# Optimization experiments

Measured on AMD Instinct MI355X. Metric: run time of the kernel, lower is better.

The kernel has to match this reference:

```python
import jax, jax.numpy as jnp
import numpy as np

DIM = 512
TEMB_DIM = 512
NUM_HEADS = 16
WS = 16  # window_size
N = WS * WS
B = 256


def _relative_position_index(ws: int) -> np.ndarray:
    """Swin-style relative position index, shape [ws*ws, ws*ws], values in [0, (2ws-1)^2)."""
    coords = np.stack(np.meshgrid(np.arange(ws), np.arange(ws), indexing='ij'))  # [2, ws, ws]
    flat = coords.reshape(2, -1)                                                  # [2, N]
    rel = flat[:, :, None] - flat[:, None, :]                                     # [2, N, N]
    rel = rel.transpose(1, 2, 0).copy()                                           # [N, N, 2]
    rel[:, :, 0] += ws - 1
    rel[:, :, 1] += ws - 1
    rel[:, :, 0] *= 2 * ws - 1
    return rel.sum(-1).astype(np.int32)


def setup_inputs() -> dict:
    key = jax.random.key(0)
    ks = jax.random.split(key, 8)
    lin = lambda k, fan_in, shape: jax.random.normal(k, shape, jnp.float32) * (1.0 / np.sqrt(fan_in))
    return {
        'x': jax.random.normal(ks[0], (B, N, DIM), jnp.float32),
        'temb': jax.random.normal(ks[1], (B, TEMB_DIM), jnp.float32),
        'qkv_w': lin(ks[2], DIM, (DIM, 3 * DIM)),
        'qkv_b': jnp.zeros((3 * DIM,), jnp.float32),
        'temb_w': lin(ks[3], TEMB_DIM, (TEMB_DIM, 3 * DIM)),
        'temb_b': jnp.zeros((3 * DIM,), jnp.float32),
        'rpb_table': jax.random.normal(ks[4], ((2 * WS - 1) ** 2, NUM_HEADS), jnp.float32) * 0.02,
        'proj_w': lin(ks[5], DIM, (DIM, DIM)),
        'proj_b': jnp.zeros((DIM,), jnp.float32),
        'rp_index': jnp.asarray(_relative_position_index(WS)),
    }


def reference(x, temb, qkv_w, qkv_b, temb_w, temb_b, rpb_table, proj_w, proj_b, rp_index):
    Bq, Nq, C = x.shape
    H = NUM_HEADS
    hd = C // H
    # qkv with time-embedding modulation: [B, N, 3C]
    qkv = x @ qkv_w + qkv_b + (temb @ temb_w + temb_b)[:, None, :]
    qkv = qkv.reshape(Bq, Nq, 3, H, hd).transpose(2, 0, 3, 1, 4)  # [3, B, H, N, hd]
    q, k, v = qkv[0], qkv[1], qkv[2]
    # relative position bias: [H, N, N]
    bias = rpb_table[rp_index.reshape(-1)].reshape(Nq, Nq, H).transpose(2, 0, 1)
    scale = 1.0 / jnp.sqrt(jnp.asarray(hd, x.dtype))  # SDPA default scale
    scores = jnp.einsum('bhqd,bhkd->bhqk', q, k) * scale + bias[None]
    attn = jax.nn.softmax(scores, axis=-1)
    out = jnp.einsum('bhqk,bhkd->bhqd', attn, v)       # [B, H, N, hd]
    out = out.transpose(0, 2, 1, 3).reshape(Bq, Nq, C)
    return out @ proj_w + proj_b
```

## Files before the change

### kernel.cpp

```cpp
#include <hip/hip_runtime.h>
#include <hip/hip_bf16.h>

#define B_ 256
#define N_ 256
#define H_ 16
#define SCALE2_ 0.25504526484f
#define LOG2E_ 1.4426950408889634f

typedef __attribute__((ext_vector_type(8))) short short8;
typedef __attribute__((ext_vector_type(4))) float f32x4v;
typedef unsigned int u32;

#define GLOAD16(gptr, lptr)                                                        \
  __builtin_amdgcn_global_load_lds((const __attribute__((address_space(1))) u32*)(gptr), \
                                   (__attribute__((address_space(3))) u32*)(lptr), 16, 0, 0)

static __device__ __forceinline__ unsigned cvt_pk_bf16(float lo, float hi) {
  unsigned r;
  asm("v_cvt_pk_bf16_f32 %0, %1, %2" : "=v"(r) : "v"(lo), "v"(hi));
  return r;
}

__global__ __launch_bounds__(512)
void prep_kernel(const float* __restrict__ temb, const float* __restrict__ temb_w,
                 const float* __restrict__ temb_b, const float* __restrict__ qkv_b,
                 float* __restrict__ tm,
                 const float* __restrict__ x, unsigned* __restrict__ xb16,
                 const float* __restrict__ qkv_w, unsigned short* __restrict__ qkv_wT,
                 const float* __restrict__ proj_w, unsigned short* __restrict__ proj_wT) {
  __shared__ __align__(16) char lbuf[17024];
  const int blk = blockIdx.x;
  const int t = threadIdx.x;

  if (blk < 256) {
    float* ts = (float*)lbuf;
    const int b = blk;
    ts[t] = temb[(size_t)b * 512 + t];
    __syncthreads();
    float a0 = temb_b[t] + qkv_b[t];
    float a1 = temb_b[t + 512] + qkv_b[t + 512];
    float a2 = temb_b[t + 1024] + qkv_b[t + 1024];
#pragma unroll 4
    for (int k = 0; k < 512; ++k) {
      const float tv = ts[k];
      const float* wr = temb_w + (size_t)k * 1536 + t;
      a0 += tv * wr[0];
      a1 += tv * wr[512];
      a2 += tv * wr[1024];
    }
    float* o = tm + (size_t)b * 1536 + t;
    o[0] = a0; o[512] = a1; o[1024] = a2;
  } else if (blk < 1280) {
    const int n8 = (B_ * N_ * 512) / 8;
    int i = (blk - 256) * 512 + t;
    for (; i < n8; i += 1024 * 512) {
      const float4* p = reinterpret_cast<const float4*>(x + (size_t)i * 8);
      float4 a = p[0], b4 = p[1];
      uint4 vv = make_uint4(cvt_pk_bf16(a.x, a.y), cvt_pk_bf16(a.z, a.w),
                            cvt_pk_bf16(b4.x, b4.y), cvt_pk_bf16(b4.z, b4.w));
      *reinterpret_cast<uint4*>(xb16 + (size_t)i * 4) = vv;
    }
  } else {
    const float* src; unsigned short* dst; int ncols, k0, n0;
    if (blk < 1472) {
      const int idx = blk - 1280;
      src = qkv_w; dst = qkv_wT; ncols = 1536;
      k0 = (idx / 12) << 5; n0 = (idx % 12) << 7;
    } else {
      const int idx = blk - 1472;
      src = proj_w; dst = proj_wT; ncols = 512;
      k0 = (idx >> 2) << 5; n0 = (idx & 3) << 7;
    }
    float (*tile)[133] = (float (*)[133])lbuf;
    {
      const int kk = t >> 4, c0 = (t & 15) << 3;
      const float* s = src + (size_t)(k0 + kk) * ncols + n0 + c0;
      float4 v0 = *reinterpret_cast<const float4*>(s);
      float4 v1 = *reinterpret_cast<const float4*>(s + 4);
      tile[kk][c0 + 0] = v0.x; tile[kk][c0 + 1] = v0.y; tile[kk][c0 + 2] = v0.z; tile[kk][c0 + 3] = v0.w;
      tile[kk][c0 + 4] = v1.x; tile[kk][c0 + 5] = v1.y; tile[kk][c0 + 6] = v1.z; tile[kk][c0 + 7] = v1.w;
    }
    __syncthreads();
    {
      const int nn = t >> 2, ck = (t & 3) << 3;
      uint4 vv = make_uint4(cvt_pk_bf16(tile[ck + 0][nn], tile[ck + 1][nn]),
                            cvt_pk_bf16(tile[ck + 2][nn], tile[ck + 3][nn]),
                            cvt_pk_bf16(tile[ck + 4][nn], tile[ck + 5][nn]),
                            cvt_pk_bf16(tile[ck + 6][nn], tile[ck + 7][nn]));
      *reinterpret_cast<uint4*>(dst + (size_t)(n0 + nn) * 512 + k0 + ck) = vv;
    }
  }
}

__global__ __launch_bounds__(512, 4)
void fused_attn_kernel(const unsigned short* __restrict__ xb16,
                       const unsigned short* __restrict__ wT,
                       const float* __restrict__ rpb,
                       const float* __restrict__ tm,
                       unsigned short* __restrict__ attn_out) {
  __shared__ __align__(16) char smem[67584];
  short* xs     = (short*)smem;
  short* ksp    = (short*)(smem + 16384);
  short* vTs    = (short*)(smem + 32768);
  short* wstage = (short*)(smem + 49152);
  float* biasT  = (float*)(smem + 49152);

  const int u = blockIdx.x;
  const int bh = ((u & 7) << 9) | (u >> 3);
  const int b = bh >> 4, h = bh & 15;
  const int tid = threadIdx.x;
  const int w = tid >> 6, l = tid & 63;
  const int l16 = l & 15, g = l >> 4;
  const int gsw8 = (g ^ ((l16 >> 1) & 3)) << 3;
  const int lrow = l >> 2;
  const int lcol = (((l & 3) ^ ((l >> 3) & 3)) << 3);

  const unsigned short* xsrc0 = xb16 + (size_t)(b * 256 + w * 16 + lrow) * 512 + lcol;
  const unsigned short* xsrc1 = xsrc0 + (size_t)128 * 512;
  const int row96 = w * 16 + lrow;
  const unsigned short* wsrc = wT + (size_t)((row96 >> 5) * 512 + h * 32 + (row96 & 31)) * 512 + lcol;

  f32x4v acc[2][6];
#pragma unroll
  for (int mt = 0; mt < 2; ++mt)
#pragma unroll
    for (int nt = 0; nt < 6; ++nt) acc[mt][nt] = (f32x4v)(0.0f);

  auto stage = [&](int t, int bufi) {
    const int k0 = t << 5;
    GLOAD16(xsrc0 + k0, xs + bufi * 8192 + w * 512);
    GLOAD16(xsrc1 + k0, xs + bufi * 8192 + (8 + w) * 512);
    if (w < 6) GLOAD16(wsrc + k0, wstage + bufi * 3072 + w * 512);
  };
  stage(0, 0);
#pragma unroll
  for (int t = 0; t < 16; ++t) {
    const int buf = t % 3;
    if (t < 15) {
      stage(t + 1, (t + 1) % 3);
      if (w < 6) asm volatile("s_waitcnt vmcnt(3)" ::: "memory");
      else       asm volatile("s_waitcnt vmcnt(2)" ::: "memory");
    } else {
      asm volatile("s_waitcnt vmcnt(0)" ::: "memory");
    }
    __builtin_amdgcn_sched_barrier(0);
    __builtin_amdgcn_s_barrier();
    __builtin_amdgcn_sched_barrier(0);
    short* xb = xs + buf * 8192;
    short* wb = wstage + buf * 3072;
    short8 af[2], bfr[6];
#pragma unroll
    for (int mt = 0; mt < 2; ++mt)
      af[mt] = *reinterpret_cast<short8*>(&xb[(w * 32 + mt * 16 + l16) * 32 + gsw8]);
#pragma unroll
    for (int nt = 0; nt < 6; ++nt)
      bfr[nt] = *reinterpret_cast<short8*>(&wb[(nt * 16 + l16) * 32 + gsw8]);
#pragma unroll
    for (int mt = 0; mt < 2; ++mt)
#pragma unroll
      for (int nt = 0; nt < 6; ++nt)
        acc[mt][nt] = __builtin_amdgcn_mfma_f32_16x16x32_bf16(af[mt], bfr[nt], acc[mt][nt], 0, 0, 0);
  }
  __syncthreads();

  const float* tmb = tm + (size_t)b * 1536 + h * 32;
#pragma unroll
  for (int nt = 0; nt < 6; ++nt) {
    const int prt = nt >> 1;
    const int d = ((nt & 1) << 4) + l16;
    const float tmv = tmb[(prt << 9) + d];
#pragma unroll
    for (int mt = 0; mt < 2; ++mt) {
      const int r0 = w * 32 + mt * 16 + g * 4;
      float v0 = acc[mt][nt][0] + tmv, v1 = acc[mt][nt][1] + tmv;
      float v2 = acc[mt][nt][2] + tmv, v3 = acc[mt][nt][3] + tmv;
      if (prt == 0) { v0 *= SCALE2_; v1 *= SCALE2_; v2 *= SCALE2_; v3 *= SCALE2_; }
      const u32 p01 = cvt_pk_bf16(v0, v1);
      const u32 p23 = cvt_pk_bf16(v2, v3);
      if (prt != 2) {
        short* dst = (prt == 0) ? xs : ksp;
        const int unit01 = ((d >> 3) ^ ((r0 >> 1) & 3)) << 3;
        const int base = r0 * 32 + unit01 + (d & 7);
        dst[base]            = (short)p01;
        dst[base + 32]       = (short)(p01 >> 16);
        dst[(base + 64) ^ 8] = (short)p23;
        dst[(base + 96) ^ 8] = (short)(p23 >> 16);
      } else {
#pragma unroll
        for (int j = 0; j < 4; ++j) {
          const int key = r0 + j;
          const int vcol = ((key >> 5) << 5) | (((key & 15) << 1) | ((key >> 4) & 1));
          const int unit = ((vcol >> 3) ^ (d & 7));
          const u32 pk = (j < 2) ? p01 : p23;
          vTs[d * 256 + (unit << 3) + (vcol & 7)] = (short)(pk >> ((j & 1) << 4));
        }
      }
    }
  }
  for (int e = tid; e < 961; e += 512) biasT[e] = rpb[e * 16 + h] * LOG2E_;
  __syncthreads();

  short8 bq[2];
#pragma unroll
  for (int mt = 0; mt < 2; ++mt)
    bq[mt] = *reinterpret_cast<short8*>(&xs[(w * 32 + mt * 16 + l16) * 32 + gsw8]);

  const int bcol = l16 - (g << 2) + 15;
  const int brow0 = w * 2 + 15;

  f32x4v bp_prev;
#pragma unroll
  for (int j = 0; j < 4; ++j) bp_prev[j] = biasT[(brow0 + 1) * 31 + bcol - j];

  short8 ones8;
#pragma unroll
  for (int j = 0; j < 8; ++j) ones8[j] = (short)0x3F80;

  f32x4v oacc[2][2];
  f32x4v oaccL[2];
#pragma unroll
  for (int mt = 0; mt < 2; ++mt) {
    oacc[mt][0] = (f32x4v)(0.0f);
    oacc[mt][1] = (f32x4v)(0.0f);
    oaccL[mt] = (f32x4v)(0.0f);
  }

#pragma unroll
  for (int kc = 0; kc < 8; ++kc) {
    const int kt0 = kc * 2, kt1 = kc * 2 + 1;
    short8 kf0 = *reinterpret_cast<short8*>(&ksp[(kt0 * 16 + l16) * 32 + gsw8]);
    short8 kf1 = *reinterpret_cast<short8*>(&ksp[(kt1 * 16 + l16) * 32 + gsw8]);
    f32x4v cA, cB;
    const float* brA = biasT + (brow0 - kt0) * 31 + bcol;
    const float* brB = biasT + (brow0 - kt1) * 31 + bcol;
#pragma unroll
    for (int j = 0; j < 4; ++j) { cA[j] = brA[-j]; cB[j] = brB[-j]; }
    f32x4v s00, s01, s10, s11;
    __builtin_amdgcn_s_setprio(1);
    s00 = __builtin_amdgcn_mfma_f32_16x16x32_bf16(kf0, bq[0], cA, 0, 0, 0);
    s01 = __builtin_amdgcn_mfma_f32_16x16x32_bf16(kf0, bq[1], bp_prev, 0, 0, 0);
    s10 = __builtin_amdgcn_mfma_f32_16x16x32_bf16(kf1, bq[0], cB, 0, 0, 0);
    s11 = __builtin_amdgcn_mfma_f32_16x16x32_bf16(kf1, bq[1], cA, 0, 0, 0);
    __builtin_amdgcn_s_setprio(0);
    bp_prev = cB;

    short8 pa0, pa1;
    {
      union { u32 u[4]; short8 s8; } pk0, pk1;
#pragma unroll
      for (int j = 0; j < 4; ++j) {
        pk0.u[j] = cvt_pk_bf16(exp2f(s00[j]), exp2f(s10[j]));
        pk1.u[j] = cvt_pk_bf16(exp2f(s01[j]), exp2f(s11[j]));
      }
      pa0 = pk0.s8; pa1 = pk1.s8;
    }
    short8 bv0 = *reinterpret_cast<short8*>(
        &vTs[(l16) * 256 + ((((kc * 4 + g) ^ (l16 & 7)) << 3))]);
    short8 bv1 = *reinterpret_cast<short8*>(
        &vTs[(16 + l16) * 256 + ((((kc * 4 + g) ^ (l16 & 7)) << 3))]);
    __builtin_amdgcn_s_setprio(1);
    oacc[0][0] = __builtin_amdgcn_mfma_f32_16x16x32_bf16(pa0, bv0, oacc[0][0], 0, 0, 0);
    oacc[0][1] = __builtin_amdgcn_mfma_f32_16x16x32_bf16(pa0, bv1, oacc[0][1], 0, 0, 0);
    oacc[1][0] = __builtin_amdgcn_mfma_f32_16x16x32_bf16(pa1, bv0, oacc[1][0], 0, 0, 0);
    oacc[1][1] = __builtin_amdgcn_mfma_f32_16x16x32_bf16(pa1, bv1, oacc[1][1], 0, 0, 0);
    oaccL[0]   = __builtin_amdgcn_mfma_f32_16x16x32_bf16(pa0, ones8, oaccL[0], 0, 0, 0);
    oaccL[1]   = __builtin_amdgcn_mfma_f32_16x16x32_bf16(pa1, ones8, oaccL[1], 0, 0, 0);
    __builtin_amdgcn_s_setprio(0);
  }

  float i0[4], i1[4];
#pragma unroll
  for (int j = 0; j < 4; ++j) {
    i0[j] = __builtin_amdgcn_rcpf(oaccL[0][j]);
    i1[j] = __builtin_amdgcn_rcpf(oaccL[1][j]);
  }
  short* ob = xs + w * 1024;
  const int u0 = (((l16 >> 3) ^ g) << 3) + (l16 & 7);
  const int u1 = ((((l16 >> 3) | 2) ^ g) << 3) + (l16 & 7);
  {
    const u32 a01 = cvt_pk_bf16(oacc[0][0][0] * i0[0], oacc[0][0][1] * i0[1]);
    const u32 a23 = cvt_pk_bf16(oacc[0][0][2] * i0[2], oacc[0][0][3] * i0[3]);
    const u32 b01 = cvt_pk_bf16(oacc[0][1][0] * i0[0], oacc[0][1][1] * i0[1]);
    const u32 b23 = cvt_pk_bf16(oacc[0][1][2] * i0[2], oacc[0][1][3] * i0[3]);
    const u32 c01 = cvt_pk_bf16(oacc[1][0][0] * i1[0], oacc[1][0][1] * i1[1]);
    const u32 c23 = cvt_pk_bf16(oacc[1][0][2] * i1[2], oacc[1][0][3] * i1[3]);
    const u32 d01 = cvt_pk_bf16(oacc[1][1][0] * i1[0], oacc[1][1][1] * i1[1]);
    const u32 d23 = cvt_pk_bf16(oacc[1][1][2] * i1[2], oacc[1][1][3] * i1[3]);
    const int r0 = (g << 2) * 32;
    ob[r0 + u0]       = (short)a01;  ob[r0 + 32 + u0]  = (short)(a01 >> 16);
    ob[r0 + 64 + u0]  = (short)a23;  ob[r0 + 96 + u0]  = (short)(a23 >> 16);
    ob[r0 + u1]       = (short)b01;  ob[r0 + 32 + u1]  = (short)(b01 >> 16);
    ob[r0 + 64 + u1]  = (short)b23;  ob[r0 + 96 + u1]  = (short)(b23 >> 16);
    const int r1 = r0 + 512;
    ob[r1 + u0]       = (short)c01;  ob[r1 + 32 + u0]  = (short)(c01 >> 16);
    ob[r1 + 64 + u0]  = (short)c23;  ob[r1 + 96 + u0]  = (short)(c23 >> 16);
    ob[r1 + u1]       = (short)d01;  ob[r1 + 32 + u1]  = (short)(d01 >> 16);
    ob[r1 + 64 + u1]  = (short)d23;  ob[r1 + 96 + u1]  = (short)(d23 >> 16);
  }
  unsigned short* aw = attn_out + (size_t)(b * 256 + w * 32) * 512 + h * 32;
#pragma unroll
  for (int i = 0; i < 2; ++i) {
    const int r = i * 16 + (l >> 2);
    const int cu = l & 3;
    const int su = cu ^ ((r >> 2) & 3);
    short8 vv = *reinterpret_cast<short8*>(&ob[r * 32 + (su << 3)]);
    *reinterpret_cast<short8*>(aw + (size_t)r * 512 + (cu << 3)) = vv;
  }
}

__global__ __launch_bounds__(256)
void proj_kernel(const unsigned short* __restrict__ A,
                 const unsigned short* __restrict__ BT,
                 const float* __restrict__ proj_b,
                 float* __restrict__ out) {
  __shared__ short As[2][4096];
  __shared__ short Bs[2][4096];
  const int bid0 = blockIdx.x;
  const int swz = ((bid0 & 7) << 8) | (bid0 >> 3);
  const int m0 = (swz >> 2) << 7;
  const int n0 = (swz & 3) << 7;
  const int tid = threadIdx.x;
  const int w = tid >> 6, l = tid & 63, l16 = l & 15, g = l >> 4;
  const int wr = w >> 1, wc = w & 1;
  const int gsw8 = (g ^ ((l16 >> 1) & 3)) << 3;
  const int lrow = l >> 2;
  const int lcol = (((l & 3) ^ ((l >> 3) & 3)) << 3);

  const unsigned short* asrc0 = A + (size_t)(m0 + w * 16 + lrow) * 512 + lcol;
  const unsigned short* asrc1 = asrc0 + (size_t)64 * 512;
  const unsigned short* bsrc0 = BT + (size_t)(n0 + w * 16 + lrow) * 512 + lcol;
  const unsigned short* bsrc1 = bsrc0 + (size_t)64 * 512;

  f32x4v acc[4][4];
#pragma unroll
  for (int mt = 0; mt < 4; ++mt)
#pragma unroll
    for (int nt = 0; nt < 4; ++nt) acc[mt][nt] = (f32x4v)(0.0f);

  auto stage = [&](int t, int bufi) {
    const int k0 = t << 5;
    GLOAD16(asrc0 + k0, As[bufi] + w * 512);
    GLOAD16(asrc1 + k0, As[bufi] + (4 + w) * 512);
    GLOAD16(bsrc0 + k0, Bs[bufi] + w * 512);
    GLOAD16(bsrc1 + k0, Bs[bufi] + (4 + w) * 512);
  };
  stage(0, 0);
  __syncthreads();
#pragma unroll
  for (int t = 0; t < 16; ++t) {
    const int cur = t & 1;
    if (t < 15) stage(t + 1, cur ^ 1);
    short8 af[4], bfr[4];
#pragma unroll
    for (int mt = 0; mt < 4; ++mt)
      af[mt] = *reinterpret_cast<short8*>(&As[cur][(wr * 64 + mt * 16 + l16) * 32 + gsw8]);
#pragma unroll
    for (int nt = 0; nt < 4; ++nt)
      bfr[nt] = *reinterpret_cast<short8*>(&Bs[cur][(wc * 64 + nt * 16 + l16) * 32 + gsw8]);
#pragma unroll
    for (int mt = 0; mt < 4; ++mt)
#pragma unroll
      for (int nt = 0; nt < 4; ++nt)
        acc[mt][nt] = __builtin_amdgcn_mfma_f32_16x16x32_bf16(af[mt], bfr[nt], acc[mt][nt], 0, 0, 0);
    __syncthreads();
  }
#pragma unroll
  for (int nt = 0; nt < 4; ++nt) {
    const int col = n0 + wc * 64 + nt * 16 + l16;
    const float pb = proj_b[col];
#pragma unroll
    for (int mt = 0; mt < 4; ++mt)
#pragma unroll
      for (int j = 0; j < 4; ++j)
        out[(size_t)(m0 + wr * 64 + mt * 16 + g * 4 + j) * 512 + col] = acc[mt][nt][j] + pb;
  }
}

extern "C" void kernel_launch(void* const* d_in, const int* in_sizes, int n_in,
                              void* d_out, int out_size, void* d_ws, size_t ws_size,
                              hipStream_t stream) {
  const float* x      = (const float*)d_in[0];
  const float* temb   = (const float*)d_in[1];
  const float* qkv_w  = (const float*)d_in[2];
  const float* qkv_b  = (const float*)d_in[3];
  const float* temb_w = (const float*)d_in[4];
  const float* temb_b = (const float*)d_in[5];
  const float* rpb    = (const float*)d_in[6];
  const float* proj_w = (const float*)d_in[7];
  const float* proj_b = (const float*)d_in[8];
  float* out = (float*)d_out;

  char* ws = (char*)d_ws;
  float* tm               = (float*)ws;
  unsigned short* xb16    = (unsigned short*)(ws + 1572864);
  unsigned short* qkv_wT  = (unsigned short*)(ws + 1572864 + 67108864);
  unsigned short* proj_wT = (unsigned short*)(ws + 1572864 + 67108864 + 1572864);
  unsigned short* attn_ws = (unsigned short*)(ws + 1572864 + 67108864 + 1572864 + 524288);

  prep_kernel<<<1536, 512, 0, stream>>>(temb, temb_w, temb_b, qkv_b, tm,
                                        x, (unsigned*)xb16,
                                        qkv_w, qkv_wT, proj_w, proj_wT);
  fused_attn_kernel<<<B_ * H_, 512, 0, stream>>>(xb16, qkv_wT, rpb, tm, attn_ws);
  proj_kernel<<<2048, 256, 0, stream>>>(attn_ws, proj_wT, proj_b, out);
}
```

Before: 334.0 us.

## Fuse fp32-to-bf16 conversion of x into the attention QKV GEMM loop

Removes the separate pass that converted x to a bf16 workspace copy. The attention kernel now loads fp32 x directly, converts it in registers and writes it into a double-buffered LDS tile, cutting the LDS footprint. This avoids writing and rereading the intermediate copy, but each head's block now reads the fp32 rows, doubling per-block input bytes. The proj kernel is also reordered so a waitcnt and barrier precede each prefetch instead of a trailing syncthreads.

```diff
diff --git a/kernel.cpp b/kernel.cpp
--- a/kernel.cpp
+++ b/kernel.cpp
@@ -25,7 +25,6 @@
 void prep_kernel(const float* __restrict__ temb, const float* __restrict__ temb_w,
                  const float* __restrict__ temb_b, const float* __restrict__ qkv_b,
                  float* __restrict__ tm,
-                 const float* __restrict__ x, unsigned* __restrict__ xb16,
                  const float* __restrict__ qkv_w, unsigned short* __restrict__ qkv_wT,
                  const float* __restrict__ proj_w, unsigned short* __restrict__ proj_wT) {
   __shared__ __align__(16) char lbuf[17024];
@@ -40,7 +39,7 @@
     float a0 = temb_b[t] + qkv_b[t];
     float a1 = temb_b[t + 512] + qkv_b[t + 512];
     float a2 = temb_b[t + 1024] + qkv_b[t + 1024];
-#pragma unroll 4
+#pragma unroll 8
     for (int k = 0; k < 512; ++k) {
       const float tv = ts[k];
       const float* wr = temb_w + (size_t)k * 1536 + t;
@@ -50,26 +49,16 @@
     }
     float* o = tm + (size_t)b * 1536 + t;
     o[0] = a0; o[512] = a1; o[1024] = a2;
-  } else if (blk < 1280) {
-    const int n8 = (B_ * N_ * 512) / 8;
-    int i = (blk - 256) * 512 + t;
-    for (; i < n8; i += 1024 * 512) {
-      const float4* p = reinterpret_cast<const float4*>(x + (size_t)i * 8);
-      float4 a = p[0], b4 = p[1];
-      uint4 vv = make_uint4(cvt_pk_bf16(a.x, a.y), cvt_pk_bf16(a.z, a.w),
-                            cvt_pk_bf16(b4.x, b4.y), cvt_pk_bf16(b4.z, b4.w));
-      *reinterpret_cast<uint4*>(xb16 + (size_t)i * 4) = vv;
-    }
   } else {
     const float* src; unsigned short* dst; int ncols, k0, n0;
-    if (blk < 1472) {
-      const int idx = blk - 1280;
+    const int idx = blk - 256;
+    if (idx < 192) {
       src = qkv_w; dst = qkv_wT; ncols = 1536;
       k0 = (idx / 12) << 5; n0 = (idx % 12) << 7;
     } else {
-      const int idx = blk - 1472;
+      const int i2 = idx - 192;
       src = proj_w; dst = proj_wT; ncols = 512;
-      k0 = (idx >> 2) << 5; n0 = (idx & 3) << 7;
+      k0 = (i2 >> 2) << 5; n0 = (i2 & 3) << 7;
     }
     float (*tile)[133] = (float (*)[133])lbuf;
     {
@@ -93,16 +82,16 @@
 }
 
 __global__ __launch_bounds__(512, 4)
-void fused_attn_kernel(const unsigned short* __restrict__ xb16,
+void fused_attn_kernel(const float* __restrict__ x,
                        const unsigned short* __restrict__ wT,
                        const float* __restrict__ rpb,
                        const float* __restrict__ tm,
                        unsigned short* __restrict__ attn_out) {
-  __shared__ __align__(16) char smem[67584];
+  __shared__ __align__(16) char smem[53008];
   short* xs     = (short*)smem;
   short* ksp    = (short*)(smem + 16384);
   short* vTs    = (short*)(smem + 32768);
-  short* wstage = (short*)(smem + 49152);
+  short* wstage = (short*)(smem + 32768);
   float* biasT  = (float*)(smem + 49152);
 
   const int u = blockIdx.x;
@@ -115,8 +104,12 @@
   const int lrow = l >> 2;
   const int lcol = (((l & 3) ^ ((l >> 3) & 3)) << 3);
 
-  const unsigned short* xsrc0 = xb16 + (size_t)(b * 256 + w * 16 + lrow) * 512 + lcol;
-  const unsigned short* xsrc1 = xsrc0 + (size_t)128 * 512;
+  const int xrow = w * 32 + (l >> 1);
+  const float* xsrcf = x + (size_t)(b * 256 + xrow) * 512 + ((l & 1) << 4);
+  const int cu0 = (l & 1) << 1;
+  const int un0 = ((cu0 ^ ((xrow >> 1) & 3)) << 3) + xrow * 32;
+  const int un1 = (((cu0 + 1) ^ ((xrow >> 1) & 3)) << 3) + xrow * 32;
+
   const int row96 = w * 16 + lrow;
   const unsigned short* wsrc = wT + (size_t)((row96 >> 5) * 512 + h * 32 + (row96 & 31)) * 512 + lcol;
 
@@ -126,28 +119,34 @@
 #pragma unroll
     for (int nt = 0; nt < 6; ++nt) acc[mt][nt] = (f32x4v)(0.0f);
 
-  auto stage = [&](int t, int bufi) {
-    const int k0 = t << 5;
-    GLOAD16(xsrc0 + k0, xs + bufi * 8192 + w * 512);
-    GLOAD16(xsrc1 + k0, xs + bufi * 8192 + (8 + w) * 512);
-    if (w < 6) GLOAD16(wsrc + k0, wstage + bufi * 3072 + w * 512);
-  };
-  stage(0, 0);
+  {
+    float4 xa = *reinterpret_cast<const float4*>(xsrcf);
+    float4 xb4 = *reinterpret_cast<const float4*>(xsrcf + 4);
+    float4 xc = *reinterpret_cast<const float4*>(xsrcf + 8);
+    float4 xd = *reinterpret_cast<const float4*>(xsrcf + 12);
+    if (w < 6) GLOAD16(wsrc, wstage + w * 512);
+    uint4 lo = make_uint4(cvt_pk_bf16(xa.x, xa.y), cvt_pk_bf16(xa.z, xa.w),
+                          cvt_pk_bf16(xb4.x, xb4.y), cvt_pk_bf16(xb4.z, xb4.w));
+    uint4 hi = make_uint4(cvt_pk_bf16(xc.x, xc.y), cvt_pk_bf16(xc.z, xc.w),
+                          cvt_pk_bf16(xd.x, xd.y), cvt_pk_bf16(xd.z, xd.w));
+    *reinterpret_cast<uint4*>(&xs[un0]) = lo;
+    *reinterpret_cast<uint4*>(&xs[un1]) = hi;
+  }
+  __syncthreads();
+
 #pragma unroll
   for (int t = 0; t < 16; ++t) {
-    const int buf = t % 3;
+    float4 xa, xb4, xc, xd;
     if (t < 15) {
-      stage(t + 1, (t + 1) % 3);
-      if (w < 6) asm volatile("s_waitcnt vmcnt(3)" ::: "memory");
-      else       asm volatile("s_waitcnt vmcnt(2)" ::: "memory");
-    } else {
-      asm volatile("s_waitcnt vmcnt(0)" ::: "memory");
-    }
-    __builtin_amdgcn_sched_barrier(0);
-    __builtin_amdgcn_s_barrier();
-    __builtin_amdgcn_sched_barrier(0);
-    short* xb = xs + buf * 8192;
-    short* wb = wstage + buf * 3072;
+      const int k0 = (t + 1) << 5;
+      xa = *reinterpret_cast<const float4*>(xsrcf + k0);
+      xb4 = *reinterpret_cast<const float4*>(xsrcf + k0 + 4);
+      xc = *reinterpret_cast<const float4*>(xsrcf + k0 + 8);
+      xd = *reinterpret_cast<const float4*>(xsrcf + k0 + 12);
+      if (w < 6) GLOAD16(wsrc + k0, wstage + ((t + 1) & 1) * 3072 + w * 512);
+    }
+    short* xb = xs + (t & 1) * 8192;
+    short* wb = wstage + (t & 1) * 3072;
     short8 af[2], bfr[6];
 #pragma unroll
     for (int mt = 0; mt < 2; ++mt)
@@ -160,8 +159,17 @@
 #pragma unroll
       for (int nt = 0; nt < 6; ++nt)
         acc[mt][nt] = __builtin_amdgcn_mfma_f32_16x16x32_bf16(af[mt], bfr[nt], acc[mt][nt], 0, 0, 0);
-  }
-  __syncthreads();
+    if (t < 15) {
+      short* xw = xs + ((t + 1) & 1) * 8192;
+      uint4 lo = make_uint4(cvt_pk_bf16(xa.x, xa.y), cvt_pk_bf16(xa.z, xa.w),
+                            cvt_pk_bf16(xb4.x, xb4.y), cvt_pk_bf16(xb4.z, xb4.w));
+      uint4 hi = make_uint4(cvt_pk_bf16(xc.x, xc.y), cvt_pk_bf16(xc.z, xc.w),
+                            cvt_pk_bf16(xd.x, xd.y), cvt_pk_bf16(xd.z, xd.w));
+      *reinterpret_cast<uint4*>(&xw[un0]) = lo;
+      *reinterpret_cast<uint4*>(&xw[un1]) = hi;
+    }
+    __syncthreads();
+  }
 
   const float* tmb = tm + (size_t)b * 1536 + h * 32;
 #pragma unroll
@@ -345,11 +353,14 @@
     GLOAD16(bsrc1 + k0, Bs[bufi] + (4 + w) * 512);
   };
   stage(0, 0);
-  __syncthreads();
 #pragma unroll
   for (int t = 0; t < 16; ++t) {
+    asm volatile("s_waitcnt vmcnt(0)" ::: "memory");
+    __builtin_amdgcn_sched_barrier(0);
+    __builtin_amdgcn_s_barrier();
+    __builtin_amdgcn_sched_barrier(0);
+    if (t < 15) stage(t + 1, (t + 1) & 1);
     const int cur = t & 1;
-    if (t < 15) stage(t + 1, cur ^ 1);
     short8 af[4], bfr[4];
 #pragma unroll
     for (int mt = 0; mt < 4; ++mt)
@@ -362,7 +373,6 @@
 #pragma unroll
       for (int nt = 0; nt < 4; ++nt)
         acc[mt][nt] = __builtin_amdgcn_mfma_f32_16x16x32_bf16(af[mt], bfr[nt], acc[mt][nt], 0, 0, 0);
-    __syncthreads();
   }
 #pragma unroll
   for (int nt = 0; nt < 4; ++nt) {
@@ -392,14 +402,12 @@
 
   char* ws = (char*)d_ws;
   float* tm               = (float*)ws;
-  unsigned short* xb16    = (unsigned short*)(ws + 1572864);
-  unsigned short* qkv_wT  = (unsigned short*)(ws + 1572864 + 67108864);
-  unsigned short* proj_wT = (unsigned short*)(ws + 1572864 + 67108864 + 1572864);
-  unsigned short* attn_ws = (unsigned short*)(ws + 1572864 + 67108864 + 1572864 + 524288);
-
-  prep_kernel<<<1536, 512, 0, stream>>>(temb, temb_w, temb_b, qkv_b, tm,
-                                        x, (unsigned*)xb16,
-                                        qkv_w, qkv_wT, proj_w, proj_wT);
-  fused_attn_kernel<<<B_ * H_, 512, 0, stream>>>(xb16, qkv_wT, rpb, tm, attn_ws);
+  unsigned short* qkv_wT  = (unsigned short*)(ws + 1572864);
+  unsigned short* proj_wT = (unsigned short*)(ws + 1572864 + 1572864);
+  unsigned short* attn_ws = (unsigned short*)(ws + 1572864 + 1572864 + 524288);
+
+  prep_kernel<<<512, 512, 0, stream>>>(temb, temb_w, temb_b, qkv_b, tm,
+                                       qkv_w, qkv_wT, proj_w, proj_wT);
+  fused_attn_kernel<<<B_ * H_, 512, 0, stream>>>(x, qkv_wT, rpb, tm, attn_ws);
   proj_kernel<<<2048, 256, 0, stream>>>(attn_ws, proj_wT, proj_b, out);
 }
```

New measurement: 365.7 us. +9.5%, slower.
